# Kernel tuning notes

Hardware: AMD Instinct MI355X
Metric: run time of the kernel (lower is better)

The kernel has to match this reference:

```python
import jax, jax.numpy as jnp
import numpy as np

K = 3  # num_stacks
T = 2  # num_layers
N_NODES = 30000
N_EDGES = 300000
F_IN = 256
F_HID = 256
F_OUT = 64


def _glorot(key, shape):
    fan_in, fan_out = shape[-2], shape[-1]
    s = jnp.sqrt(6.0 / (fan_in + fan_out))
    return jax.random.uniform(key, shape, jnp.float32, -s, s)


def setup_inputs() -> dict:
    key = jax.random.key(0)
    ks = jax.random.split(key, 12)
    x = jax.random.normal(ks[0], (N_NODES, F_IN), jnp.float32)
    edge_index = jax.random.randint(ks[1], (2, N_EDGES), 0, N_NODES, jnp.int64)
    return {
        "x": x,
        "edge_index": edge_index,
        # conv1 (in -> hidden), shared weights across layers
        "init_w1": _glorot(ks[2], (K, F_IN, F_HID)),
        "w1": _glorot(ks[3], (K, F_HID, F_HID)),
        "root_w1": _glorot(ks[4], (K, F_IN, F_HID)),
        "bias1": jnp.zeros((K, 1, F_HID), jnp.float32),
        # conv2 (hidden -> out)
        "init_w2": _glorot(ks[5], (K, F_HID, F_OUT)),
        "w2": _glorot(ks[6], (K, F_OUT, F_OUT)),
        "root_w2": _glorot(ks[7], (K, F_HID, F_OUT)),
        "bias2": jnp.zeros((K, 1, F_OUT), jnp.float32),
    }


def _gcn_norm(edge_index, num_nodes):
    # gcn_norm with add_self_loops=False: deg over destination (col)
    row, col = edge_index[0], edge_index[1]
    deg = jax.ops.segment_sum(jnp.ones((edge_index.shape[1],), jnp.float32), col,
                              num_segments=num_nodes)
    dis = jnp.where(deg > 0, jax.lax.rsqrt(jnp.maximum(deg, 1.0)), 0.0)
    return dis[row] * dis[col]


def _propagate(h, row, col, norm, num_nodes):
    # h: [K, N, F] -> sum over incoming edges of norm * h[src]
    msg = norm[None, :, None] * h[:, row]  # [K, E, F]
    return jax.vmap(lambda m: jax.ops.segment_sum(m, col, num_segments=num_nodes))(msg)


def _arma_conv(x, row, col, norm, init_w, w, root_w, bias, act):
    # shared_weights=True: weight/root_weight reused for every layer t>0 / t
    num_nodes = x.shape[0]
    root = jnp.einsum('nf,kfo->kno', x, root_w) + bias  # [K, N, F_out]
    h = jnp.einsum('nf,kfo->kno', x, init_w)
    for t in range(T):
        if t > 0:
            h = jnp.einsum('kno,kop->knp', h, w)
        h = _propagate(h, row, col, norm, num_nodes)
        h = act(h + root)
    return h.mean(axis=0)  # mean over stacks -> [N, F_out]


def reference(x, edge_index, init_w1, w1, root_w1, bias1, init_w2, w2, root_w2, bias2):
    # eval mode: all dropouts are identity
    row, col = edge_index[0], edge_index[1]
    norm = _gcn_norm(edge_index, x.shape[0])
    h = _arma_conv(x, row, col, norm, init_w1, w1, root_w1, bias1, jax.nn.relu)
    h = jax.nn.relu(h)
    h = _arma_conv(h, row, col, norm, init_w2, w2, root_w2, bias2, lambda t: t)
    return jax.nn.log_softmax(h, axis=1)
```

## Files before the change

### kernel.cpp

```cpp
#include <hip/hip_runtime.h>
#include <hip/hip_bf16.h>

#define NN 30000
#define NE 300000

typedef unsigned short u16;
typedef unsigned int u32;
typedef unsigned long long u64;
typedef short s16x8 __attribute__((ext_vector_type(8)));
typedef float f32x4 __attribute__((ext_vector_type(4)));

__device__ __forceinline__ float bf2f(u16 u) { return __uint_as_float(((u32)u) << 16); }
__device__ __forceinline__ u16 f2bf(float f) {
    u32 u = __float_as_uint(f);
    u32 r = (u + 0x7FFFu + ((u >> 16) & 1u)) >> 16;
    return (u16)r;
}

__global__ void hist_kernel(const int* __restrict__ col, int* __restrict__ deg) {
    int e = blockIdx.x * blockDim.x + threadIdx.x;
    if (e < NE) atomicAdd(&deg[col[e]], 1);
}

__global__ void dis_kernel(const int* __restrict__ deg, float* __restrict__ dis) {
    int i = blockIdx.x * blockDim.x + threadIdx.x;
    if (i < NN) {
        int d = deg[i];
        dis[i] = d > 0 ? rsqrtf((float)d) : 0.0f;
    }
}

__global__ __launch_bounds__(1024) void scan_kernel(const int* __restrict__ deg,
                                                    int* __restrict__ rowptr) {
    __shared__ int buf[1024];
    __shared__ int carry_s;
    if (threadIdx.x == 0) { carry_s = 0; rowptr[0] = 0; }
    __syncthreads();
    for (int base = 0; base < NN; base += 1024) {
        int i = base + (int)threadIdx.x;
        int v = (i < NN) ? deg[i] : 0;
        buf[threadIdx.x] = v;
        __syncthreads();
        for (int off = 1; off < 1024; off <<= 1) {
            int t = (threadIdx.x >= (unsigned)off) ? buf[threadIdx.x - off] : 0;
            __syncthreads();
            buf[threadIdx.x] += t;
            __syncthreads();
        }
        int carry = carry_s;
        if (i < NN) rowptr[i + 1] = carry + buf[threadIdx.x];
        __syncthreads();
        if (threadIdx.x == 1023) carry_s = carry + buf[1023];
        __syncthreads();
    }
}

__global__ void scatter_kernel(const int* __restrict__ row, const int* __restrict__ col,
                               const int* __restrict__ rowptr, int* __restrict__ cursor,
                               const float* __restrict__ dis, int* __restrict__ src,
                               float* __restrict__ ew) {
    int e = blockIdx.x * blockDim.x + threadIdx.x;
    if (e < NE) {
        int c = col[e];
        int r = row[e];
        int pos = rowptr[c] + atomicAdd(&cursor[c], 1);
        src[pos] = r;
        ew[pos] = dis[r] * dis[c];
    }
}

__global__ void f2bf_vec(const float* __restrict__ in, u16* __restrict__ out, long n4) {
    long i = (long)blockIdx.x * blockDim.x + threadIdx.x;
    if (i < n4) {
        float4 v = *(const float4*)&in[i * 4];
        u16 o[4] = { f2bf(v.x), f2bf(v.y), f2bf(v.z), f2bf(v.w) };
        *(u64*)&out[i * 4] = *(u64*)o;
    }
}

__global__ void prep_w(const float* __restrict__ W, u16* __restrict__ Wt, int Kd, int Od) {
    long idx = (long)blockIdx.x * blockDim.x + threadIdx.x;
    long total = 3L * Kd * Od;
    if (idx < total) {
        int kk = idx % Kd;
        long rest = idx / Kd;
        int o = rest % Od;
        int k = rest / Od;
        Wt[idx] = f2bf(W[((long)k * Kd + kk) * Od + o]);
    }
}

template<int U64W>
__global__ __launch_bounds__(U64W < 64 ? 64 : U64W) void prop_node(
    const u16* __restrict__ h, u16* __restrict__ out,
    const int* __restrict__ rowptr, const int* __restrict__ src,
    const float* __restrict__ ew)
{
    int n = blockIdx.x;
    int t = threadIdx.x;
    if (U64W < 64 && t >= U64W) return;
    int beg = rowptr[n], end = rowptr[n + 1];
    const u64* hu = (const u64*)h;
    float a0 = 0.f, a1 = 0.f, a2 = 0.f, a3 = 0.f;
    int e = beg;
    int s = 0; float w = 0.f;
    if (e < end) { s = src[e]; w = ew[e]; }
    while (e < end) {
        int e2 = e + 1; int s2 = 0; float w2 = 0.f;
        if (e2 < end) { s2 = src[e2]; w2 = ew[e2]; }
        u64 v = hu[(size_t)s * U64W + t];
        a0 += w * bf2f((u16)v);
        a1 += w * bf2f((u16)(v >> 16));
        a2 += w * bf2f((u16)(v >> 32));
        a3 += w * bf2f((u16)(v >> 48));
        e = e2; s = s2; w = w2;
    }
    u16 o[4] = { f2bf(a0), f2bf(a1), f2bf(a2), f2bf(a3) };
    ((u64*)out)[(size_t)n * U64W + t] = *(u64*)o;
}

template<int BN, int HAS_ADD, int HAS_BIAS, int RELU>
__global__ __launch_bounds__(256) void gemm_one(
    const u16* __restrict__ A, int pitchA, int stOffA,
    const u16* __restrict__ Wt, const float* __restrict__ bias,
    const u16* __restrict__ addend, u16* __restrict__ out,
    int M, int O, int K)
{
    constexpr int NJ = BN / 32;
    constexpr int NB = (BN * 4) / 256;
    const int m0 = blockIdx.x * 128;
    const int o0 = blockIdx.y * BN;
    const int st = blockIdx.z;
    const u16* Ak = A + (size_t)st * stOffA;
    const u16* Wk = Wt + (size_t)st * O * K;
    __shared__ u16 As[128][40];
    __shared__ u16 Bs[BN][40];
    const int tid = threadIdx.x;
    const int lane = tid & 63, wave = tid >> 6;
    const int wrow = wave >> 1, wcol = wave & 1;
    const int l15 = lane & 15, l4 = lane >> 4;
    f32x4 acc[4][NJ] = {};
    for (int kt = 0; kt < K; kt += 32) {
#pragma unroll
        for (int hh = 0; hh < 2; hh++) {
            int c = tid + hh * 256;
            int row = c >> 2, kc = (c & 3) * 8;
            int gr = m0 + row;
            uint4 v = {0, 0, 0, 0};
            if (gr < M) v = *(const uint4*)&Ak[(size_t)gr * pitchA + kt + kc];
            *(uint4*)&As[row][kc] = v;
        }
#pragma unroll
        for (int hh = 0; hh < NB; hh++) {
            int c = tid + hh * 256;
            int row = c >> 2, kc = (c & 3) * 8;
            *(uint4*)&Bs[row][kc] = *(const uint4*)&Wk[(size_t)(o0 + row) * K + kt + kc];
        }
        __syncthreads();
        s16x8 bfr[NJ];
#pragma unroll
        for (int j = 0; j < NJ; j++)
            bfr[j] = *(const s16x8*)&Bs[wcol * (BN / 2) + j * 16 + l15][l4 * 8];
#pragma unroll
        for (int i = 0; i < 4; i++) {
            s16x8 a = *(const s16x8*)&As[wrow * 64 + i * 16 + l15][l4 * 8];
#pragma unroll
            for (int j = 0; j < NJ; j++)
                acc[i][j] = __builtin_amdgcn_mfma_f32_16x16x32_bf16(a, bfr[j], acc[i][j], 0, 0, 0);
        }
        __syncthreads();
    }
#pragma unroll
    for (int i = 0; i < 4; i++)
#pragma unroll
        for (int j = 0; j < NJ; j++) {
            int cg = o0 + wcol * (BN / 2) + j * 16 + l15;
            float bv = HAS_BIAS ? bias[st * O + cg] : 0.0f;
#pragma unroll
            for (int q = 0; q < 4; q++) {
                int rg = m0 + wrow * 64 + i * 16 + l4 * 4 + q;
                if (rg < M) {
                    float v = acc[i][j][q] + bv;
                    if (HAS_ADD) v += bf2f(addend[((size_t)rg * 3 + st) * O + cg]);
                    if (RELU) v = fmaxf(v, 0.0f);
                    out[((size_t)rg * 3 + st) * O + cg] = f2bf(v);
                }
            }
        }
}

template<int RELU2>
__global__ __launch_bounds__(256) void gemm_dual(
    const u16* __restrict__ A1, const u16* __restrict__ A2,
    const u16* __restrict__ W1, const u16* __restrict__ W2,
    const float* __restrict__ bias,
    u16* __restrict__ out1, u16* __restrict__ out2,
    int M, int O, int K)
{
    const int m0 = blockIdx.x * 128;
    const int o0 = blockIdx.y * 64;
    const int st = blockIdx.z;
    const u16* W1k = W1 + (size_t)st * O * K;
    const u16* W2k = W2 + (size_t)st * O * K;
    __shared__ u16 As[128][40];
    __shared__ u16 Bs[64][40];
    const int tid = threadIdx.x;
    const int lane = tid & 63, wave = tid >> 6;
    const int wrow = wave >> 1, wcol = wave & 1;
    const int l15 = lane & 15, l4 = lane >> 4;

    f32x4 acc1[4][2] = {};
    for (int kt = 0; kt < K; kt += 32) {
#pragma unroll
        for (int hh = 0; hh < 2; hh++) {
            int c = tid + hh * 256;
            int row = c >> 2, kc = (c & 3) * 8;
            int gr = m0 + row;
            uint4 v = {0, 0, 0, 0};
            if (gr < M) v = *(const uint4*)&A1[(size_t)gr * K + kt + kc];
            *(uint4*)&As[row][kc] = v;
        }
        { int row = tid >> 2, kc = (tid & 3) * 8;
          *(uint4*)&Bs[row][kc] = *(const uint4*)&W1k[(size_t)(o0 + row) * K + kt + kc]; }
        __syncthreads();
        s16x8 b0 = *(const s16x8*)&Bs[wcol * 32 + l15][l4 * 8];
        s16x8 b1 = *(const s16x8*)&Bs[wcol * 32 + 16 + l15][l4 * 8];
#pragma unroll
        for (int i = 0; i < 4; i++) {
            s16x8 a = *(const s16x8*)&As[wrow * 64 + i * 16 + l15][l4 * 8];
            acc1[i][0] = __builtin_amdgcn_mfma_f32_16x16x32_bf16(a, b0, acc1[i][0], 0, 0, 0);
            acc1[i][1] = __builtin_amdgcn_mfma_f32_16x16x32_bf16(a, b1, acc1[i][1], 0, 0, 0);
        }
        __syncthreads();
    }
#pragma unroll
    for (int j = 0; j < 2; j++) {
        int cg = o0 + wcol * 32 + j * 16 + l15;
        float bv = bias[st * O + cg];
#pragma unroll
        for (int i = 0; i < 4; i++)
#pragma unroll
            for (int q = 0; q < 4; q++) {
                acc1[i][j][q] += bv;
                int rg = m0 + wrow * 64 + i * 16 + l4 * 4 + q;
                if (rg < M) out1[((size_t)rg * 3 + st) * O + cg] = f2bf(acc1[i][j][q]);
            }
    }
    f32x4 acc2[4][2] = {};
    for (int kt = 0; kt < K; kt += 32) {
#pragma unroll
        for (int hh = 0; hh < 2; hh++) {
            int c = tid + hh * 256;
            int row = c >> 2, kc = (c & 3) * 8;
            int gr = m0 + row;
            uint4 v = {0, 0, 0, 0};
            if (gr < M) v = *(const uint4*)&A2[(size_t)gr * K + kt + kc];
            *(uint4*)&As[row][kc] = v;
        }
        { int row = tid >> 2, kc = (tid & 3) * 8;
          *(uint4*)&Bs[row][kc] = *(const uint4*)&W2k[(size_t)(o0 + row) * K + kt + kc]; }
        __syncthreads();
        s16x8 b0 = *(const s16x8*)&Bs[wcol * 32 + l15][l4 * 8];
        s16x8 b1 = *(const s16x8*)&Bs[wcol * 32 + 16 + l15][l4 * 8];
#pragma unroll
        for (int i = 0; i < 4; i++) {
            s16x8 a = *(const s16x8*)&As[wrow * 64 + i * 16 + l15][l4 * 8];
            acc2[i][0] = __builtin_amdgcn_mfma_f32_16x16x32_bf16(a, b0, acc2[i][0], 0, 0, 0);
            acc2[i][1] = __builtin_amdgcn_mfma_f32_16x16x32_bf16(a, b1, acc2[i][1], 0, 0, 0);
        }
        __syncthreads();
    }
#pragma unroll
    for (int j = 0; j < 2; j++) {
        int cg = o0 + wcol * 32 + j * 16 + l15;
#pragma unroll
        for (int i = 0; i < 4; i++)
#pragma unroll
            for (int q = 0; q < 4; q++) {
                int rg = m0 + wrow * 64 + i * 16 + l4 * 4 + q;
                if (rg < M) {
                    float v = acc2[i][j][q] + acc1[i][j][q];
                    if (RELU2) v = fmaxf(v, 0.0f);
                    out2[((size_t)rg * 3 + st) * O + cg] = f2bf(v);
                }
            }
    }
}

__global__ void mean3_256(const u16* __restrict__ h, u16* __restrict__ out) {
    long idx = (long)blockIdx.x * blockDim.x + threadIdx.x;
    const long total = (long)NN * 128;
    if (idx >= total) return;
    long n = idx >> 7; int t = (int)(idx & 127);
    const u32* hu = (const u32*)h;
    u32 a = hu[(n * 3 + 0) * 128 + t], b = hu[(n * 3 + 1) * 128 + t], c = hu[(n * 3 + 2) * 128 + t];
    float lo = (bf2f((u16)a) + bf2f((u16)b) + bf2f((u16)c)) * (1.0f / 3.0f);
    float hi = (bf2f((u16)(a >> 16)) + bf2f((u16)(b >> 16)) + bf2f((u16)(c >> 16))) * (1.0f / 3.0f);
    ((u32*)out)[idx] = (u32)f2bf(lo) | ((u32)f2bf(hi) << 16);
}

__global__ __launch_bounds__(64) void final_ls(const u16* __restrict__ g, float* __restrict__ out) {
    int n = blockIdx.x;
    int f = threadIdx.x;
    long b0 = (long)n * 192 + f;
    float v = (bf2f(g[b0]) + bf2f(g[b0 + 64]) + bf2f(g[b0 + 128])) * (1.0f / 3.0f);
    float m = v;
    for (int off = 32; off; off >>= 1) m = fmaxf(m, __shfl_xor(m, off, 64));
    float s = expf(v - m);
    for (int off = 32; off; off >>= 1) s += __shfl_xor(s, off, 64);
    out[(long)n * 64 + f] = v - m - logf(s);
}

extern "C" void kernel_launch(void* const* d_in, const int* in_sizes, int n_in,
                              void* d_out, int out_size, void* d_ws, size_t ws_size,
                              hipStream_t stream) {
    const float* x = (const float*)d_in[0];
    const int* ei = (const int*)d_in[1];
    const float* init_w1 = (const float*)d_in[2];
    const float* w1 = (const float*)d_in[3];
    const float* root_w1 = (const float*)d_in[4];
    const float* bias1 = (const float*)d_in[5];
    const float* init_w2 = (const float*)d_in[6];
    const float* w2 = (const float*)d_in[7];
    const float* root_w2 = (const float*)d_in[8];
    const float* bias2 = (const float*)d_in[9];
    float* out = (float*)d_out;
    (void)ws_size; (void)n_in; (void)in_sizes; (void)out_size;

    char* ws = (char*)d_ws;
    size_t off = 0;
    auto alloc = [&](size_t bytes) -> void* {
        void* p = ws + off;
        off += (bytes + 255) & ~(size_t)255;
        return p;
    };
    int* deg = (int*)alloc(NN * 4);
    int* rowptr = (int*)alloc((NN + 1) * 4);
    int* cursor = (int*)alloc(NN * 4);
    int* srcb = (int*)alloc((size_t)NE * 4);
    float* ewb = (float*)alloc((size_t)NE * 4);
    float* dis = (float*)alloc(NN * 4);
    u16* iw1t = (u16*)alloc((size_t)3 * 256 * 256 * 2);
    u16* w1t = (u16*)alloc((size_t)3 * 256 * 256 * 2);
    u16* rw1t = (u16*)alloc((size_t)3 * 256 * 256 * 2);
    u16* iw2t = (u16*)alloc((size_t)3 * 64 * 256 * 2);
    u16* rw2t = (u16*)alloc((size_t)3 * 64 * 256 * 2);
    u16* w2t = (u16*)alloc((size_t)3 * 64 * 64 * 2);
    u16* xb = (u16*)alloc((size_t)NN * 256 * 2);
    u16* bufR = (u16*)alloc((size_t)NN * 3 * 256 * 2);
    u16* bufH = (u16*)alloc((size_t)NN * 3 * 256 * 2);
    u16* bufP = (u16*)alloc((size_t)NN * 3 * 256 * 2);
    u16* px = bufP;
    u16* hmean = bufP;
    u16* pm = xb;
    u16* root2 = bufR;
    u16* g1 = bufR + (size_t)3 * NN * 64;
    u16* pg1 = bufR + (size_t)6 * NN * 64;
    u16* g2 = bufR + (size_t)9 * NN * 64;

    const int* e_row = ei;
    const int* e_col = ei + NE;

    hipMemsetAsync(deg, 0, NN * 4, stream);
    hipMemsetAsync(cursor, 0, NN * 4, stream);

    hist_kernel<<<(NE + 255) / 256, 256, 0, stream>>>(e_col, deg);
    dis_kernel<<<(NN + 255) / 256, 256, 0, stream>>>(deg, dis);
    scan_kernel<<<1, 1024, 0, stream>>>(deg, rowptr);
    scatter_kernel<<<(NE + 255) / 256, 256, 0, stream>>>(e_row, e_col, rowptr, cursor, dis, srcb, ewb);

    f2bf_vec<<<(NN * 256 / 4 + 255) / 256, 256, 0, stream>>>(x, xb, (long)NN * 256 / 4);
    prep_w<<<(3 * 256 * 256 + 255) / 256, 256, 0, stream>>>(init_w1, iw1t, 256, 256);
    prep_w<<<(3 * 256 * 256 + 255) / 256, 256, 0, stream>>>(w1, w1t, 256, 256);
    prep_w<<<(3 * 256 * 256 + 255) / 256, 256, 0, stream>>>(root_w1, rw1t, 256, 256);
    prep_w<<<(3 * 64 * 256 + 255) / 256, 256, 0, stream>>>(init_w2, iw2t, 256, 64);
    prep_w<<<(3 * 64 * 256 + 255) / 256, 256, 0, stream>>>(root_w2, rw2t, 256, 64);
    prep_w<<<(3 * 64 * 64 + 255) / 256, 256, 0, stream>>>(w2, w2t, 64, 64);

    const int MB = (NN + 127) / 128;

    prop_node<64><<<NN, 64, 0, stream>>>(xb, px, rowptr, srcb, ewb);
    gemm_dual<1><<<dim3(MB, 4, 3), 256, 0, stream>>>(xb, px, rw1t, iw1t, bias1,
                                                     bufR, bufH, NN, 256, 256);
    prop_node<192><<<NN, 192, 0, stream>>>(bufH, bufP, rowptr, srcb, ewb);
    gemm_one<128, 1, 0, 1><<<dim3(MB, 2, 3), 256, 0, stream>>>(
        bufP, 768, 256, w1t, nullptr, bufR, bufH, NN, 256, 256);
    mean3_256<<<(int)(((long)NN * 128 + 255) / 256), 256, 0, stream>>>(bufH, hmean);

    prop_node<64><<<NN, 64, 0, stream>>>(hmean, pm, rowptr, srcb, ewb);
    gemm_dual<0><<<dim3(MB, 1, 3), 256, 0, stream>>>(hmean, pm, rw2t, iw2t, bias2,
                                                     root2, g1, NN, 64, 256);
    prop_node<48><<<NN, 64, 0, stream>>>(g1, pg1, rowptr, srcb, ewb);
    gemm_one<64, 1, 0, 0><<<dim3(MB, 1, 3), 256, 0, stream>>>(
        pg1, 192, 64, w2t, nullptr, root2, g2, NN, 64, 64);

    final_ls<<<NN, 64, 0, stream>>>(g2, out);
}
```

Before: 548.1 us.

## Fuse dual GEMM K-loops and flatten grid for row-block locality

The dual GEMM now loads both A operands and both weight tiles in one K-loop and runs the two MFMA chains interleaved, instead of two sequential passes. Both GEMM kernels also switch to a 1D grid in which the output-column and stack indices vary fastest, so blocks that share the same A rows run close together and can reuse them from L2. The aim is fewer barriers, more independent MFMA work per loop iteration and better cache reuse of the large activation matrices. In exchange, shared memory per block doubles and register pressure rises from holding both accumulator sets at once, which could lower occupancy.

```diff
diff --git a/kernel.cpp b/kernel.cpp
--- a/kernel.cpp
+++ b/kernel.cpp
@@ -124,13 +124,16 @@
     const u16* __restrict__ A, int pitchA, int stOffA,
     const u16* __restrict__ Wt, const float* __restrict__ bias,
     const u16* __restrict__ addend, u16* __restrict__ out,
-    int M, int O, int K)
+    int M, int O, int K, int NY)
 {
     constexpr int NJ = BN / 32;
     constexpr int NB = (BN * 4) / 256;
-    const int m0 = blockIdx.x * 128;
-    const int o0 = blockIdx.y * BN;
-    const int st = blockIdx.z;
+    const int nyz = NY * 3;
+    const int yz = blockIdx.x % nyz;
+    const int mb = blockIdx.x / nyz;
+    const int m0 = mb * 128;
+    const int o0 = (yz % NY) * BN;
+    const int st = yz / NY;
     const u16* Ak = A + (size_t)st * stOffA;
     const u16* Wk = Wt + (size_t)st * O * K;
     __shared__ u16 As[128][40];
@@ -195,41 +198,58 @@
     const u16* __restrict__ W1, const u16* __restrict__ W2,
     const float* __restrict__ bias,
     u16* __restrict__ out1, u16* __restrict__ out2,
-    int M, int O, int K)
+    int M, int O, int K, int NY)
 {
-    const int m0 = blockIdx.x * 128;
-    const int o0 = blockIdx.y * 64;
-    const int st = blockIdx.z;
+    const int nyz = NY * 3;
+    const int yz = blockIdx.x % nyz;
+    const int mb = blockIdx.x / nyz;
+    const int m0 = mb * 128;
+    const int o0 = (yz % NY) * 64;
+    const int st = yz / NY;
     const u16* W1k = W1 + (size_t)st * O * K;
     const u16* W2k = W2 + (size_t)st * O * K;
-    __shared__ u16 As[128][40];
-    __shared__ u16 Bs[64][40];
+    __shared__ u16 As1[128][40];
+    __shared__ u16 As2[128][40];
+    __shared__ u16 Bs1[64][40];
+    __shared__ u16 Bs2[64][40];
     const int tid = threadIdx.x;
     const int lane = tid & 63, wave = tid >> 6;
     const int wrow = wave >> 1, wcol = wave & 1;
     const int l15 = lane & 15, l4 = lane >> 4;
+    const int srow = tid >> 2;
+    const int skoff = (tid & 3) * 8;
 
     f32x4 acc1[4][2] = {};
+    f32x4 acc2[4][2] = {};
     for (int kt = 0; kt < K; kt += 32) {
 #pragma unroll
         for (int hh = 0; hh < 2; hh++) {
             int c = tid + hh * 256;
             int row = c >> 2, kc = (c & 3) * 8;
             int gr = m0 + row;
-            uint4 v = {0, 0, 0, 0};
-            if (gr < M) v = *(const uint4*)&A1[(size_t)gr * K + kt + kc];
-            *(uint4*)&As[row][kc] = v;
-        }
-        { int row = tid >> 2, kc = (tid & 3) * 8;
-          *(uint4*)&Bs[row][kc] = *(const uint4*)&W1k[(size_t)(o0 + row) * K + kt + kc]; }
-        __syncthreads();
-        s16x8 b0 = *(const s16x8*)&Bs[wcol * 32 + l15][l4 * 8];
-        s16x8 b1 = *(const s16x8*)&Bs[wcol * 32 + 16 + l15][l4 * 8];
+            uint4 v1 = {0, 0, 0, 0}, v2 = {0, 0, 0, 0};
+            if (gr < M) {
+                v1 = *(const uint4*)&A1[(size_t)gr * K + kt + kc];
+                v2 = *(const uint4*)&A2[(size_t)gr * K + kt + kc];
+            }
+            *(uint4*)&As1[row][kc] = v1;
+            *(uint4*)&As2[row][kc] = v2;
+        }
+        *(uint4*)&Bs1[srow][skoff] = *(const uint4*)&W1k[(size_t)(o0 + srow) * K + kt + skoff];
+        *(uint4*)&Bs2[srow][skoff] = *(const uint4*)&W2k[(size_t)(o0 + srow) * K + kt + skoff];
+        __syncthreads();
+        s16x8 b10 = *(const s16x8*)&Bs1[wcol * 32 + l15][l4 * 8];
+        s16x8 b11 = *(const s16x8*)&Bs1[wcol * 32 + 16 + l15][l4 * 8];
+        s16x8 b20 = *(const s16x8*)&Bs2[wcol * 32 + l15][l4 * 8];
+        s16x8 b21 = *(const s16x8*)&Bs2[wcol * 32 + 16 + l15][l4 * 8];
 #pragma unroll
         for (int i = 0; i < 4; i++) {
-            s16x8 a = *(const s16x8*)&As[wrow * 64 + i * 16 + l15][l4 * 8];
-            acc1[i][0] = __builtin_amdgcn_mfma_f32_16x16x32_bf16(a, b0, acc1[i][0], 0, 0, 0);
-            acc1[i][1] = __builtin_amdgcn_mfma_f32_16x16x32_bf16(a, b1, acc1[i][1], 0, 0, 0);
+            s16x8 a1 = *(const s16x8*)&As1[wrow * 64 + i * 16 + l15][l4 * 8];
+            s16x8 a2 = *(const s16x8*)&As2[wrow * 64 + i * 16 + l15][l4 * 8];
+            acc1[i][0] = __builtin_amdgcn_mfma_f32_16x16x32_bf16(a1, b10, acc1[i][0], 0, 0, 0);
+            acc1[i][1] = __builtin_amdgcn_mfma_f32_16x16x32_bf16(a1, b11, acc1[i][1], 0, 0, 0);
+            acc2[i][0] = __builtin_amdgcn_mfma_f32_16x16x32_bf16(a2, b20, acc2[i][0], 0, 0, 0);
+            acc2[i][1] = __builtin_amdgcn_mfma_f32_16x16x32_bf16(a2, b21, acc2[i][1], 0, 0, 0);
         }
         __syncthreads();
     }
@@ -241,47 +261,13 @@
         for (int i = 0; i < 4; i++)
 #pragma unroll
             for (int q = 0; q < 4; q++) {
-                acc1[i][j][q] += bv;
-                int rg = m0 + wrow * 64 + i * 16 + l4 * 4 + q;
-                if (rg < M) out1[((size_t)rg * 3 + st) * O + cg] = f2bf(acc1[i][j][q]);
-            }
-    }
-    f32x4 acc2[4][2] = {};
-    for (int kt = 0; kt < K; kt += 32) {
-#pragma unroll
-        for (int hh = 0; hh < 2; hh++) {
-            int c = tid + hh * 256;
-            int row = c >> 2, kc = (c & 3) * 8;
-            int gr = m0 + row;
-            uint4 v = {0, 0, 0, 0};
-            if (gr < M) v = *(const uint4*)&A2[(size_t)gr * K + kt + kc];
-            *(uint4*)&As[row][kc] = v;
-        }
-        { int row = tid >> 2, kc = (tid & 3) * 8;
-          *(uint4*)&Bs[row][kc] = *(const uint4*)&W2k[(size_t)(o0 + row) * K + kt + kc]; }
-        __syncthreads();
-        s16x8 b0 = *(const s16x8*)&Bs[wcol * 32 + l15][l4 * 8];
-        s16x8 b1 = *(const s16x8*)&Bs[wcol * 32 + 16 + l15][l4 * 8];
-#pragma unroll
-        for (int i = 0; i < 4; i++) {
-            s16x8 a = *(const s16x8*)&As[wrow * 64 + i * 16 + l15][l4 * 8];
-            acc2[i][0] = __builtin_amdgcn_mfma_f32_16x16x32_bf16(a, b0, acc2[i][0], 0, 0, 0);
-            acc2[i][1] = __builtin_amdgcn_mfma_f32_16x16x32_bf16(a, b1, acc2[i][1], 0, 0, 0);
-        }
-        __syncthreads();
-    }
-#pragma unroll
-    for (int j = 0; j < 2; j++) {
-        int cg = o0 + wcol * 32 + j * 16 + l15;
-#pragma unroll
-        for (int i = 0; i < 4; i++)
-#pragma unroll
-            for (int q = 0; q < 4; q++) {
                 int rg = m0 + wrow * 64 + i * 16 + l4 * 4 + q;
                 if (rg < M) {
-                    float v = acc2[i][j][q] + acc1[i][j][q];
-                    if (RELU2) v = fmaxf(v, 0.0f);
-                    out2[((size_t)rg * 3 + st) * O + cg] = f2bf(v);
+                    float o1 = acc1[i][j][q] + bv;
+                    out1[((size_t)rg * 3 + st) * O + cg] = f2bf(o1);
+                    float o2 = acc2[i][j][q] + o1;
+                    if (RELU2) o2 = fmaxf(o2, 0.0f);
+                    out2[((size_t)rg * 3 + st) * O + cg] = f2bf(o2);
                 }
             }
     }
@@ -380,19 +366,19 @@
     const int MB = (NN + 127) / 128;
 
     prop_node<64><<<NN, 64, 0, stream>>>(xb, px, rowptr, srcb, ewb);
-    gemm_dual<1><<<dim3(MB, 4, 3), 256, 0, stream>>>(xb, px, rw1t, iw1t, bias1,
-                                                     bufR, bufH, NN, 256, 256);
+    gemm_dual<1><<<MB * 12, 256, 0, stream>>>(xb, px, rw1t, iw1t, bias1,
+                                              bufR, bufH, NN, 256, 256, 4);
     prop_node<192><<<NN, 192, 0, stream>>>(bufH, bufP, rowptr, srcb, ewb);
-    gemm_one<128, 1, 0, 1><<<dim3(MB, 2, 3), 256, 0, stream>>>(
-        bufP, 768, 256, w1t, nullptr, bufR, bufH, NN, 256, 256);
+    gemm_one<128, 1, 0, 1><<<MB * 6, 256, 0, stream>>>(
+        bufP, 768, 256, w1t, nullptr, bufR, bufH, NN, 256, 256, 2);
     mean3_256<<<(int)(((long)NN * 128 + 255) / 256), 256, 0, stream>>>(bufH, hmean);
 
     prop_node<64><<<NN, 64, 0, stream>>>(hmean, pm, rowptr, srcb, ewb);
-    gemm_dual<0><<<dim3(MB, 1, 3), 256, 0, stream>>>(hmean, pm, rw2t, iw2t, bias2,
-                                                     root2, g1, NN, 64, 256);
+    gemm_dual<0><<<MB * 3, 256, 0, stream>>>(hmean, pm, rw2t, iw2t, bias2,
+                                             root2, g1, NN, 64, 256, 1);
     prop_node<48><<<NN, 64, 0, stream>>>(g1, pg1, rowptr, srcb, ewb);
-    gemm_one<64, 1, 0, 0><<<dim3(MB, 1, 3), 256, 0, stream>>>(
-        pg1, 192, 64, w2t, nullptr, root2, g2, NN, 64, 64);
+    gemm_one<64, 1, 0, 0><<<MB * 3, 256, 0, stream>>>(
+        pg1, 192, 64, w2t, nullptr, root2, g2, NN, 64, 64, 1);
 
     final_ls<<<NN, 64, 0, stream>>>(g2, out);
 }
```

Result: no change. 549.2 us (+0.2%).
